# Kernel tuning notes

Measured on AMD Instinct MI355X. Metric: run time of the kernel, lower is better.

## Reference

```python
import jax, jax.numpy as jnp
import numpy as np

B, T, C, H = 2, 2048, 2048, 16
HD = C // H  # 128
WINDOW = 2048


def setup_inputs() -> dict:
    key = jax.random.key(0)
    k0, k1, k2 = jax.random.split(key, 3)
    s = 0.02  # GPT-2 style init scale
    return {
        "x": jax.random.normal(k0, (B, T, C), jnp.float32),
        "w_attn": jax.random.normal(k1, (3 * C, C), jnp.float32) * s,
        "b_attn": jnp.zeros((3 * C,), jnp.float32),
        "w_proj": jax.random.normal(k2, (C, C), jnp.float32) * s,
        "b_proj": jnp.zeros((C,), jnp.float32),
    }


def reference(x, w_attn, b_attn, w_proj, b_proj):
    Bb, Tt, Cc = x.shape
    # fused qkv projection (torch Linear: y = x @ W^T + b)
    qkv = x @ w_attn.T + b_attn                       # [B, T, 3C]
    q, k, v = jnp.split(qkv, 3, axis=2)

    def to_heads(t):
        return t.reshape(Bb, Tt, H, HD).transpose(0, 2, 1, 3)  # [B, H, T, HD]

    q, k, v = to_heads(q), to_heads(k), to_heads(v)
    K = k.shape[2]  # kv length (== T, no past_kv)

    attn = jnp.einsum('bhqd,bhkd->bhqk', q, k) / jnp.sqrt(jnp.float32(HD))
    # Faithful to source: mask[:, :, T-1:T, :K] — single tril row T-1 broadcast
    # over all query positions (for prefill K==T this row is all ones).
    mask_row = jnp.arange(K) <= (Tt - 1)              # [K] bool
    attn = jnp.where(mask_row[None, None, None, :], attn, -jnp.inf)
    weights = jax.nn.softmax(attn, axis=-1)            # [B, H, T, K]
    # dropout p=0.0 (eval): identity
    ctx = jnp.einsum('bhqk,bhkd->bhqd', weights, v)    # [B, H, T, HD]
    ctx = ctx.transpose(0, 2, 1, 3).reshape(Bb, Tt, Cc)
    out = ctx @ w_proj.T + b_proj                      # [B, T, C]
    return (out, k, v)  # (context, present_kv)
```

## Files before the change

kernel.cpp:

```cpp
#include <hip/hip_runtime.h>
#include <hip/hip_bf16.h>
#include <cstdint>
#include <cstddef>
#include <cmath>

typedef __attribute__((ext_vector_type(8))) short short8;
typedef __attribute__((ext_vector_type(4))) short bf16x4;
typedef __attribute__((ext_vector_type(4))) float f32x4;

static constexpr int BB = 2, T = 2048, C = 2048, H = 16, HD = 128;
static constexpr int M = BB * T;
static constexpr size_t BTC = (size_t)BB * T * C;

__device__ __forceinline__ short f2bf(float f) {
    union { float f; uint32_t u; } v; v.f = f;
    uint32_t u = v.u;
    uint32_t r = (u + 0x7fffu + ((u >> 16) & 1u)) >> 16;
    return (short)r;
}

__device__ __forceinline__ short f2bf_fast(float f) {
    __hip_bfloat16 h = __float2bfloat16(f);
    return *reinterpret_cast<short*>(&h);
}

__device__ __forceinline__ void gl_lds16(const void* g, void* l) {
    __builtin_amdgcn_global_load_lds(
        (const __attribute__((address_space(1))) unsigned int*)g,
        (__attribute__((address_space(3))) unsigned int*)l, 16, 0, 0);
}

__global__ void cvt_bf16(const float* __restrict__ in, short* __restrict__ out, int n) {
    int i = (blockIdx.x * 256 + threadIdx.x) * 8;
    if (i >= n) return;
    float4 a = *(const float4*)(in + i);
    float4 b = *(const float4*)(in + i + 4);
    short8 o;
    o[0] = f2bf(a.x); o[1] = f2bf(a.y); o[2] = f2bf(a.z); o[3] = f2bf(a.w);
    o[4] = f2bf(b.x); o[5] = f2bf(b.y); o[6] = f2bf(b.z); o[7] = f2bf(b.w);
    *(short8*)(out + i) = o;
}

__launch_bounds__(512, 2)
__global__ void gemm_qkv(const short* __restrict__ A, const short* __restrict__ Bw,
                         const float* __restrict__ bias, float* __restrict__ outF,
                         short* __restrict__ q_ws, short* __restrict__ k_ws) {
    extern __shared__ char lds[];
    constexpr int K = 2048, NKT = K / 64;
    constexpr int BUFSZ = 65536;

    int bid = blockIdx.x;
    int swz = (bid & 7) * 48 + (bid >> 3);
    int by = swz / 24, bx = swz % 24;
    int row0 = by * 256, col0 = bx * 256;

    int t = threadIdx.x, w = t >> 6, l = t & 63;
    int lr = l & 15, lg = l >> 4;
    int wr = w >> 2, wc = w & 3;

    const char* srcb[8];
    int dstoff[8];
#pragma unroll
    for (int c = 0; c < 8; c++) {
        bool isA = c < 4;
        int coff = (isA ? c : c - 4) * 8192 + t * 16;
        int row = coff >> 7;
        int colb = (coff & 127) ^ ((row & 7) << 4);
        srcb[c] = isA ? (const char*)A + (size_t)(row0 + row) * (K * 2) + colb
                      : (const char*)Bw + (size_t)(col0 + row) * (K * 2) + colb;
        dstoff[c] = (isA ? 0 : 32768) + coff;
    }

    f32x4 acc[8][4] = {};

#pragma unroll
    for (int c = 0; c < 8; c++) gl_lds16(srcb[c], lds + dstoff[c]);
#pragma unroll
    for (int c = 0; c < 8; c++) gl_lds16(srcb[c] + 128, lds + BUFSZ + dstoff[c]);
    asm volatile("s_waitcnt vmcnt(8)" ::: "memory");
    __builtin_amdgcn_s_barrier();

    for (int kt = 0; kt < NKT; kt++) {
        char* base = lds + (kt & 1) * BUFSZ;
        const char* Bbase = base + 32768;
        int koff = (kt + 2) * 128;
        bool pf = (kt + 2 < NKT);

        short8 bfr[4][2];
#pragma unroll
        for (int p = 0; p < 4; p++) {
            short8 af[2][2];
#pragma unroll
            for (int mi2 = 0; mi2 < 2; mi2++) {
                int row = wr * 128 + p * 32 + mi2 * 16 + lr;
#pragma unroll
                for (int ks = 0; ks < 2; ks++)
                    af[mi2][ks] = *(const short8*)(base + row * 128 +
                                  ((ks * 64 + lg * 16) ^ ((row & 7) << 4)));
            }
            if (p == 0) {
#pragma unroll
                for (int ni = 0; ni < 4; ni++) {
                    int row = wc * 64 + ni * 16 + lr;
#pragma unroll
                    for (int ks = 0; ks < 2; ks++)
                        bfr[ni][ks] = *(const short8*)(Bbase + row * 128 +
                                      ((ks * 64 + lg * 16) ^ ((row & 7) << 4)));
                }
            }
            __builtin_amdgcn_s_barrier();
            __builtin_amdgcn_s_setprio(1);
#pragma unroll
            for (int ks = 0; ks < 2; ks++)
#pragma unroll
                for (int mi2 = 0; mi2 < 2; mi2++)
#pragma unroll
                    for (int ni = 0; ni < 4; ni++)
                        acc[p * 2 + mi2][ni] = __builtin_amdgcn_mfma_f32_16x16x32_bf16(
                            af[mi2][ks], bfr[ni][ks], acc[p * 2 + mi2][ni], 0, 0, 0);
            __builtin_amdgcn_s_setprio(0);
            __builtin_amdgcn_s_barrier();

            if (pf) {
                if (p == 0) { gl_lds16(srcb[4] + koff, base + dstoff[4]);
                              gl_lds16(srcb[5] + koff, base + dstoff[5]); }
                if (p == 1) { gl_lds16(srcb[0] + koff, base + dstoff[0]);
                              gl_lds16(srcb[2] + koff, base + dstoff[2]); }
                if (p == 2) { gl_lds16(srcb[6] + koff, base + dstoff[6]);
                              gl_lds16(srcb[7] + koff, base + dstoff[7]); }
                if (p == 3) { gl_lds16(srcb[1] + koff, base + dstoff[1]);
                              gl_lds16(srcb[3] + koff, base + dstoff[3]); }
            }
            if (p == 3) {
                if (pf) asm volatile("s_waitcnt vmcnt(8)" ::: "memory");
                else    asm volatile("s_waitcnt vmcnt(0)" ::: "memory");
                __builtin_amdgcn_s_barrier();
            }
        }
    }

#pragma unroll
    for (int mi = 0; mi < 8; mi++) {
        int gr0 = row0 + wr * 128 + mi * 16 + lg * 4;
#pragma unroll
        for (int ni = 0; ni < 4; ni++) {
            int gc = col0 + wc * 64 + ni * 16 + lr;
            float bv = bias[gc];
            int sec = gc >> 11, cc = gc & 2047;
            int h = cc >> 7, d = cc & 127;
#pragma unroll
            for (int r = 0; r < 4; r++) {
                float val = acc[mi][ni][r] + bv;
                int gr = gr0 + r;
                int b = gr >> 11, tt = gr & 2047;
                size_t idx = ((size_t)(b * H + h) * T + tt) * HD + d;
                if (sec == 0) {
                    q_ws[idx] = f2bf(val);
                } else if (sec == 1) {
                    outF[BTC + idx] = val;
                    k_ws[idx] = f2bf(val);
                } else {
                    outF[2 * BTC + idx] = val;
                }
            }
        }
    }
}

template<int NI, int EPI, int NBX>
__launch_bounds__(512, 2)
__global__ void gemm8p(const short* __restrict__ A, const short* __restrict__ Bw,
                       const float* __restrict__ bias, float* __restrict__ outF,
                       short* __restrict__ q_ws, short* __restrict__ k_ws, int Ndim) {
    extern __shared__ char lds[];
    constexpr int K = 2048, NKT = K / 64;
    constexpr int NCH = 4 + NI;
    constexpr int BUFSZ = 32768 + NI * 8192;

    int bid = blockIdx.x;
    int nwg = gridDim.x;
    int swz = (bid & 7) * (nwg >> 3) + (bid >> 3);
    int by = swz / NBX, bx = swz % NBX;
    int row0 = by * 256, col0 = bx * (NI * 64);

    int t = threadIdx.x, w = t >> 6, l = t & 63;
    int lr = l & 15, lg = l >> 4;
    int wr = w >> 2, wc = w & 3;

    const char* srcb[NCH];
    int dstoff[NCH];
#pragma unroll
    for (int c = 0; c < NCH; c++) {
        bool isA = c < 4;
        int coff = (isA ? c : c - 4) * 8192 + t * 16;
        int row = coff >> 7;
        int colb = (coff & 127) ^ ((row & 7) << 4);
        srcb[c] = isA ? (const char*)A + (size_t)(row0 + row) * (K * 2) + colb
                      : (const char*)Bw + (size_t)(col0 + row) * (K * 2) + colb;
        dstoff[c] = (isA ? 0 : 32768) + coff;
    }

    f32x4 acc[8][NI] = {};

#pragma unroll
    for (int c = 0; c < NCH; c++) gl_lds16(srcb[c], lds + dstoff[c]);
#pragma unroll
    for (int c = 0; c < NCH; c++) gl_lds16(srcb[c] + 128, lds + BUFSZ + dstoff[c]);
    asm volatile("s_waitcnt vmcnt(%0)" :: "n"(NCH) : "memory");
    __builtin_amdgcn_s_barrier();

    for (int kt = 0; kt < NKT; kt++) {
        char* base = lds + (kt & 1) * BUFSZ;
        const char* Bbase = base + 32768;
        int koff = (kt + 2) * 128;
        bool pf = (kt + 2 < NKT);

        short8 bfr[NI][2];
#pragma unroll
        for (int p = 0; p < 4; p++) {
            short8 af[2][2];
#pragma unroll
            for (int mi2 = 0; mi2 < 2; mi2++) {
                int row = wr * 128 + p * 32 + mi2 * 16 + lr;
#pragma unroll
                for (int ks = 0; ks < 2; ks++)
                    af[mi2][ks] = *(const short8*)(base + row * 128 +
                                  ((ks * 64 + lg * 16) ^ ((row & 7) << 4)));
            }
            if (p == 0) {
#pragma unroll
                for (int ni = 0; ni < NI; ni++) {
                    int row = wc * (NI * 16) + ni * 16 + lr;
#pragma unroll
                    for (int ks = 0; ks < 2; ks++)
                        bfr[ni][ks] = *(const short8*)(Bbase + row * 128 +
                                      ((ks * 64 + lg * 16) ^ ((row & 7) << 4)));
                }
            }
            __builtin_amdgcn_s_barrier();
            __builtin_amdgcn_s_setprio(1);
#pragma unroll
            for (int ks = 0; ks < 2; ks++)
#pragma unroll
                for (int mi2 = 0; mi2 < 2; mi2++)
#pragma unroll
                    for (int ni = 0; ni < NI; ni++)
                        acc[p * 2 + mi2][ni] = __builtin_amdgcn_mfma_f32_16x16x32_bf16(
                            af[mi2][ks], bfr[ni][ks], acc[p * 2 + mi2][ni], 0, 0, 0);
            __builtin_amdgcn_s_setprio(0);
            __builtin_amdgcn_s_barrier();

            if (p == 0 && pf) {
#pragma unroll
                for (int c = 4; c < NCH; c++) gl_lds16(srcb[c] + koff, base + dstoff[c]);
            }
            if (p == 1 && pf) {
                gl_lds16(srcb[0] + koff, base + dstoff[0]);
                gl_lds16(srcb[2] + koff, base + dstoff[2]);
            }
            if (p == 3) {
                if (pf) {
                    gl_lds16(srcb[1] + koff, base + dstoff[1]);
                    gl_lds16(srcb[3] + koff, base + dstoff[3]);
                    asm volatile("s_waitcnt vmcnt(%0)" :: "n"(NCH) : "memory");
                } else {
                    asm volatile("s_waitcnt vmcnt(0)" ::: "memory");
                }
                __builtin_amdgcn_s_barrier();
            }
        }
    }

#pragma unroll
    for (int mi = 0; mi < 8; mi++) {
        int gr0 = row0 + wr * 128 + mi * 16 + lg * 4;
#pragma unroll
        for (int ni = 0; ni < NI; ni++) {
            int gc = col0 + wc * (NI * 16) + ni * 16 + lr;
            float bv = bias[gc];
#pragma unroll
            for (int r = 0; r < 4; r++)
                outF[(size_t)(gr0 + r) * Ndim + gc] = acc[mi][ni][r] + bv;
        }
    }
}

__global__ void vtrans(const float* __restrict__ vin, short* __restrict__ vT) {
    __shared__ float tile[64 * 65];
    int blk = blockIdx.x;
    int bh = blk >> 6, rem = blk & 63;
    int t0 = (rem >> 1) * 64, d0 = (rem & 1) * 64;
    const float* src = vin + (size_t)bh * T * HD;
    short* dst = vT + (size_t)bh * HD * T;
    int t = threadIdx.x;
#pragma unroll
    for (int i = 0; i < 16; i++) {
        int idx = i * 256 + t;
        int r = idx >> 6, c = idx & 63;
        tile[r * 65 + c] = src[(size_t)(t0 + r) * HD + d0 + c];
    }
    __syncthreads();
#pragma unroll
    for (int i = 0; i < 16; i++) {
        int idx = i * 256 + t;
        int rd = idx >> 6, cc = idx & 63;
        dst[(size_t)(d0 + rd) * T + t0 + cc] = f2bf(tile[cc * 65 + rd]);
    }
}

__launch_bounds__(256, 2)
__global__ void attn_fwd(const short* __restrict__ q_ws, const short* __restrict__ k_ws,
                         const short* __restrict__ vT_ws, short* __restrict__ ctx) {
    __shared__ __attribute__((aligned(16))) char K_lds[2][64 * 256];
    __shared__ __attribute__((aligned(16))) char VT_lds[2][128 * 128];
    __shared__ __attribute__((aligned(16))) char P_lds[4][16 * 128];

    int bid = blockIdx.x;
    int blk = (bid & 7) * 64 + (bid >> 3);
    int bh = blk >> 4;
    int q0 = (blk & 15) * 128;
    int b = bh >> 4, h = bh & 15;
    int t = threadIdx.x, w = t >> 6, l = t & 63;
    int lr = l & 15, lg = l >> 4;
    int sw = (lr & 7) << 4;

    short8 qf[2][4];
#pragma unroll
    for (int qt = 0; qt < 2; qt++) {
        const short* Qp = q_ws + ((size_t)bh * T + q0 + w * 32 + qt * 16 + lr) * HD;
#pragma unroll
        for (int c = 0; c < 4; c++) qf[qt][c] = *(const short8*)(Qp + c * 32 + lg * 8);
    }

    const char* Kp = (const char*)(k_ws + (size_t)bh * T * HD);
    const short* VTp = vT_ws + (size_t)bh * HD * T;
    char* Pc = P_lds[w];

    const float SC = 0.12753123813884803f;
    float m[2] = {-INFINITY, -INFINITY}, lsum[2] = {0.f, 0.f};
    f32x4 acc[2][8] = {};

    auto STAGE = [&](int kt, int bsel) {
#pragma unroll
        for (int i = 0; i < 4; i++) {
            int off = i * 4096 + t * 16;
            int swzK = off ^ (((off >> 8) & 7) << 4);
            gl_lds16(Kp + (size_t)kt * 16384 + swzK, K_lds[bsel] + off);
            int swzV = off ^ (((off >> 7) & 7) << 4);
            int row = swzV >> 7, cole = (swzV & 127) >> 1;
            gl_lds16(VTp + (size_t)row * T + kt * 64 + cole, VT_lds[bsel] + off);
        }
    };

    STAGE(0, 0);
    asm volatile("s_waitcnt vmcnt(0)" ::: "memory");
    __syncthreads();

    for (int kt = 0; kt < T / 64; kt++) {
        int cur = kt & 1;
        if (kt + 1 < T / 64) STAGE(kt + 1, cur ^ 1);
        const char* Kc = K_lds[cur];
        const char* Vc = VT_lds[cur];

        f32x4 sacc[2][4] = {};
#pragma unroll
        for (int kj = 0; kj < 4; kj++) {
            int rowb = (kj * 16 + lr) * 256;
#pragma unroll
            for (int c = 0; c < 4; c++) {
                short8 kf = *(const short8*)(Kc + ((rowb + c * 64 + lg * 16) ^ sw));
                sacc[0][kj] = __builtin_amdgcn_mfma_f32_16x16x32_bf16(kf, qf[0][c], sacc[0][kj], 0, 0, 0);
                sacc[1][kj] = __builtin_amdgcn_mfma_f32_16x16x32_bf16(kf, qf[1][c], sacc[1][kj], 0, 0, 0);
            }
        }

#pragma unroll
        for (int qt = 0; qt < 2; qt++) {
            float t0 = fmaxf(fmaxf(sacc[qt][0][0], sacc[qt][0][1]), fmaxf(sacc[qt][0][2], sacc[qt][0][3]));
            float t1 = fmaxf(fmaxf(sacc[qt][1][0], sacc[qt][1][1]), fmaxf(sacc[qt][1][2], sacc[qt][1][3]));
            float t2 = fmaxf(fmaxf(sacc[qt][2][0], sacc[qt][2][1]), fmaxf(sacc[qt][2][2], sacc[qt][2][3]));
            float t3 = fmaxf(fmaxf(sacc[qt][3][0], sacc[qt][3][1]), fmaxf(sacc[qt][3][2], sacc[qt][3][3]));
            float xm = fmaxf(fmaxf(t0, t1), fmaxf(t2, t3)) * SC;
            xm = fmaxf(xm, __shfl_xor(xm, 16));
            xm = fmaxf(xm, __shfl_xor(xm, 32));

            if (!__all(xm <= m[qt] + 8.0f)) {
                float mn = fmaxf(m[qt], xm);
                float al = __builtin_exp2f(m[qt] - mn);
                m[qt] = mn;
                lsum[qt] *= al;
                float ar[4];
#pragma unroll
                for (int r = 0; r < 4; r++) ar[r] = __shfl(al, lg * 4 + r);
#pragma unroll
                for (int nj = 0; nj < 8; nj++)
#pragma unroll
                    for (int r = 0; r < 4; r++) acc[qt][nj][r] *= ar[r];
            }

            float s0 = 0.f;
#pragma unroll
            for (int kj = 0; kj < 4; kj++) {
                bf16x4 pk;
#pragma unroll
                for (int r = 0; r < 4; r++) {
                    float pv = __builtin_exp2f(__builtin_fmaf(sacc[qt][kj][r], SC, -m[qt]));
                    s0 += pv;
                    pk[r] = f2bf_fast(pv);
                }
                *(bf16x4*)(Pc + ((lr * 128 + kj * 32 + lg * 8) ^ sw)) = pk;
            }
            s0 += __shfl_xor(s0, 16);
            s0 += __shfl_xor(s0, 32);
            lsum[qt] += s0;

            asm volatile("s_waitcnt lgkmcnt(0)" ::: "memory");

#pragma unroll
            for (int c2 = 0; c2 < 2; c2++) {
                short8 pf2 = *(const short8*)(Pc + ((lr * 128 + c2 * 64 + lg * 16) ^ sw));
#pragma unroll
                for (int nj = 0; nj < 8; nj++) {
                    short8 vf = *(const short8*)(Vc + (((nj * 16 + lr) * 128 + c2 * 64 + lg * 16) ^ sw));
                    acc[qt][nj] = __builtin_amdgcn_mfma_f32_16x16x32_bf16(pf2, vf, acc[qt][nj], 0, 0, 0);
                }
            }
        }

        asm volatile("s_waitcnt vmcnt(0)" ::: "memory");
        __syncthreads();
    }

#pragma unroll
    for (int qt = 0; qt < 2; qt++)
#pragma unroll
        for (int r = 0; r < 4; r++) {
            float rs = __shfl(lsum[qt], lg * 4 + r);
            float inv = 1.0f / rs;
            int tq = q0 + w * 32 + qt * 16 + lg * 4 + r;
            size_t base = ((size_t)b * T + tq) * C + h * HD;
#pragma unroll
            for (int nj = 0; nj < 8; nj++)
                ctx[base + nj * 16 + lr] = f2bf_fast(acc[qt][nj][r] * inv);
        }
}

extern "C" void kernel_launch(void* const* d_in, const int* in_sizes, int n_in,
                              void* d_out, int out_size, void* d_ws, size_t ws_size,
                              hipStream_t stream) {
    const float* x      = (const float*)d_in[0];
    const float* w_attn = (const float*)d_in[1];
    const float* b_attn = (const float*)d_in[2];
    const float* w_proj = (const float*)d_in[3];
    const float* b_proj = (const float*)d_in[4];
    float* out = (float*)d_out;

    char* ws = (char*)d_ws;
    short* x_bf  = (short*)ws;
    short* wp_bf = (short*)ws;
    short* wa_bf = (short*)(ws + 16777216);
    short* ctx   = (short*)(ws + 16777216);
    short* vT    = (short*)(ws + 41943040);

    short* q_ws = (short*)d_out;
    short* k_ws = (short*)d_out + BTC;

    hipFuncSetAttribute((const void*)gemm_qkv,
                        hipFuncAttributeMaxDynamicSharedMemorySize, 131072);
    hipFuncSetAttribute((const void*)gemm8p<2, 1, 16>,
                        hipFuncAttributeMaxDynamicSharedMemorySize, 98304);

    cvt_bf16<<<4096, 256, 0, stream>>>(x, x_bf, (int)BTC);
    cvt_bf16<<<6144, 256, 0, stream>>>(w_attn, wa_bf, 3 * C * C);

    gemm_qkv<<<384, 512, 131072, stream>>>(x_bf, wa_bf, b_attn, out, q_ws, k_ws);

    vtrans<<<2048, 256, 0, stream>>>(out + 2 * BTC, vT);
    cvt_bf16<<<2048, 256, 0, stream>>>(w_proj, wp_bf, C * C);

    attn_fwd<<<512, 256, 0, stream>>>(q_ws, k_ws, vT, ctx);

    gemm8p<2, 1, 16><<<256, 512, 98304, stream>>>(ctx, wp_bf, b_proj, out, nullptr, nullptr, 2048);
}
```

Baseline: 307.7 us.

## Retile QKV GEMM to 256x192 with 512 blocks and merge input conversions

Changes the QKV GEMM tile from 256x256 (384 blocks) to 256x192 (512 blocks), giving exactly two blocks per CU on 256 CUs instead of a partial wave. Block IDs are remapped so each group of eight shares rows and columns for L2 reuse. The per-phase barriers and staggered prefetches are replaced by a single prefetch and barrier pair per k-tile, which cuts synchronisation but may hurt overlap. The two fp32-to-bf16 conversion launches for x and w_attn are merged into one kernel to save a launch.

```diff
diff --git a/kernel.cpp b/kernel.cpp
--- a/kernel.cpp
+++ b/kernel.cpp
@@ -41,52 +41,68 @@
     *(short8*)(out + i) = o;
 }
 
+__global__ void cvt_qkv_in(const float* __restrict__ x, const float* __restrict__ wa,
+                           short* __restrict__ xb, short* __restrict__ wab) {
+    int i = (blockIdx.x * 256 + threadIdx.x) * 8;
+    const float* src;
+    short* dst;
+    if (i < (int)BTC) { src = x + i; dst = xb + i; }
+    else { src = wa + (i - (int)BTC); dst = wab + (i - (int)BTC); }
+    float4 a = *(const float4*)(src);
+    float4 b = *(const float4*)(src + 4);
+    short8 o;
+    o[0] = f2bf(a.x); o[1] = f2bf(a.y); o[2] = f2bf(a.z); o[3] = f2bf(a.w);
+    o[4] = f2bf(b.x); o[5] = f2bf(b.y); o[6] = f2bf(b.z); o[7] = f2bf(b.w);
+    *(short8*)(dst) = o;
+}
+
 __launch_bounds__(512, 2)
-__global__ void gemm_qkv(const short* __restrict__ A, const short* __restrict__ Bw,
-                         const float* __restrict__ bias, float* __restrict__ outF,
-                         short* __restrict__ q_ws, short* __restrict__ k_ws) {
+__global__ void gemm_qkv256(const short* __restrict__ A, const short* __restrict__ Bw,
+                            const float* __restrict__ bias, float* __restrict__ outF,
+                            short* __restrict__ q_ws, short* __restrict__ k_ws) {
     extern __shared__ char lds[];
     constexpr int K = 2048, NKT = K / 64;
-    constexpr int BUFSZ = 65536;
+    constexpr int BUFSZ = 57344;
 
     int bid = blockIdx.x;
-    int swz = (bid & 7) * 48 + (bid >> 3);
-    int by = swz / 24, bx = swz % 24;
-    int row0 = by * 256, col0 = bx * 256;
+    int g = bid & 7, j = bid >> 3;
+    int by = (g & 1) * 8 + (j >> 3);
+    int bx = (g >> 1) * 8 + (j & 7);
+    int row0 = by * 256, col0 = bx * 192;
 
     int t = threadIdx.x, w = t >> 6, l = t & 63;
     int lr = l & 15, lg = l >> 4;
     int wr = w >> 2, wc = w & 3;
 
-    const char* srcb[8];
-    int dstoff[8];
-#pragma unroll
-    for (int c = 0; c < 8; c++) {
+    const char* Ab = (const char*)A;
+    const char* Bb = (const char*)Bw;
+    const char* srcb[7];
+    int dstoff[7];
+#pragma unroll
+    for (int c = 0; c < 7; c++) {
         bool isA = c < 4;
         int coff = (isA ? c : c - 4) * 8192 + t * 16;
         int row = coff >> 7;
         int colb = (coff & 127) ^ ((row & 7) << 4);
-        srcb[c] = isA ? (const char*)A + (size_t)(row0 + row) * (K * 2) + colb
-                      : (const char*)Bw + (size_t)(col0 + row) * (K * 2) + colb;
+        srcb[c] = isA ? Ab + (size_t)(row0 + row) * (K * 2) + colb
+                      : Bb + (size_t)(col0 + row) * (K * 2) + colb;
         dstoff[c] = (isA ? 0 : 32768) + coff;
     }
 
-    f32x4 acc[8][4] = {};
-
-#pragma unroll
-    for (int c = 0; c < 8; c++) gl_lds16(srcb[c], lds + dstoff[c]);
-#pragma unroll
-    for (int c = 0; c < 8; c++) gl_lds16(srcb[c] + 128, lds + BUFSZ + dstoff[c]);
-    asm volatile("s_waitcnt vmcnt(8)" ::: "memory");
+    f32x4 acc[8][3] = {};
+
+#pragma unroll
+    for (int c = 0; c < 7; c++) gl_lds16(srcb[c], lds + dstoff[c]);
+#pragma unroll
+    for (int c = 0; c < 7; c++) gl_lds16(srcb[c] + 128, lds + BUFSZ + dstoff[c]);
+    asm volatile("s_waitcnt vmcnt(7)" ::: "memory");
     __builtin_amdgcn_s_barrier();
 
     for (int kt = 0; kt < NKT; kt++) {
-        char* base = lds + (kt & 1) * BUFSZ;
-        const char* Bbase = base + 32768;
-        int koff = (kt + 2) * 128;
-        bool pf = (kt + 2 < NKT);
-
-        short8 bfr[4][2];
+        const char* Abase = lds + (kt & 1) * BUFSZ;
+        const char* Bbase = Abase + 32768;
+
+        short8 bfr[3][2];
 #pragma unroll
         for (int p = 0; p < 4; p++) {
             short8 af[2][2];
@@ -95,56 +111,50 @@
                 int row = wr * 128 + p * 32 + mi2 * 16 + lr;
 #pragma unroll
                 for (int ks = 0; ks < 2; ks++)
-                    af[mi2][ks] = *(const short8*)(base + row * 128 +
+                    af[mi2][ks] = *(const short8*)(Abase + row * 128 +
                                   ((ks * 64 + lg * 16) ^ ((row & 7) << 4)));
             }
             if (p == 0) {
 #pragma unroll
-                for (int ni = 0; ni < 4; ni++) {
-                    int row = wc * 64 + ni * 16 + lr;
+                for (int ni = 0; ni < 3; ni++) {
+                    int row = wc * 48 + ni * 16 + lr;
 #pragma unroll
                     for (int ks = 0; ks < 2; ks++)
                         bfr[ni][ks] = *(const short8*)(Bbase + row * 128 +
                                       ((ks * 64 + lg * 16) ^ ((row & 7) << 4)));
                 }
             }
-            __builtin_amdgcn_s_barrier();
             __builtin_amdgcn_s_setprio(1);
 #pragma unroll
             for (int ks = 0; ks < 2; ks++)
 #pragma unroll
                 for (int mi2 = 0; mi2 < 2; mi2++)
 #pragma unroll
-                    for (int ni = 0; ni < 4; ni++)
+                    for (int ni = 0; ni < 3; ni++)
                         acc[p * 2 + mi2][ni] = __builtin_amdgcn_mfma_f32_16x16x32_bf16(
                             af[mi2][ks], bfr[ni][ks], acc[p * 2 + mi2][ni], 0, 0, 0);
             __builtin_amdgcn_s_setprio(0);
-            __builtin_amdgcn_s_barrier();
-
-            if (pf) {
-                if (p == 0) { gl_lds16(srcb[4] + koff, base + dstoff[4]);
-                              gl_lds16(srcb[5] + koff, base + dstoff[5]); }
-                if (p == 1) { gl_lds16(srcb[0] + koff, base + dstoff[0]);
-                              gl_lds16(srcb[2] + koff, base + dstoff[2]); }
-                if (p == 2) { gl_lds16(srcb[6] + koff, base + dstoff[6]);
-                              gl_lds16(srcb[7] + koff, base + dstoff[7]); }
-                if (p == 3) { gl_lds16(srcb[1] + koff, base + dstoff[1]);
-                              gl_lds16(srcb[3] + koff, base + dstoff[3]); }
-            }
-            if (p == 3) {
-                if (pf) asm volatile("s_waitcnt vmcnt(8)" ::: "memory");
-                else    asm volatile("s_waitcnt vmcnt(0)" ::: "memory");
-                __builtin_amdgcn_s_barrier();
-            }
-        }
+        }
+
+        __builtin_amdgcn_s_barrier();
+        if (kt + 2 < NKT) {
+            int koff = (kt + 2) * 128;
+            char* dbase = lds + (kt & 1) * BUFSZ;
+#pragma unroll
+            for (int c = 0; c < 7; c++) gl_lds16(srcb[c] + koff, dbase + dstoff[c]);
+            asm volatile("s_waitcnt vmcnt(7)" ::: "memory");
+        } else {
+            asm volatile("s_waitcnt vmcnt(0)" ::: "memory");
+        }
+        __builtin_amdgcn_s_barrier();
     }
 
 #pragma unroll
     for (int mi = 0; mi < 8; mi++) {
         int gr0 = row0 + wr * 128 + mi * 16 + lg * 4;
 #pragma unroll
-        for (int ni = 0; ni < 4; ni++) {
-            int gc = col0 + wc * 64 + ni * 16 + lr;
+        for (int ni = 0; ni < 3; ni++) {
+            int gc = col0 + wc * 48 + ni * 16 + lr;
             float bv = bias[gc];
             int sec = gc >> 11, cc = gc & 2047;
             int h = cc >> 7, d = cc & 127;
@@ -171,7 +181,7 @@
 __launch_bounds__(512, 2)
 __global__ void gemm8p(const short* __restrict__ A, const short* __restrict__ Bw,
                        const float* __restrict__ bias, float* __restrict__ outF,
-                       short* __restrict__ q_ws, short* __restrict__ k_ws, int Ndim) {
+                       int Ndim) {
     extern __shared__ char lds[];
     constexpr int K = 2048, NKT = K / 64;
     constexpr int NCH = 4 + NI;
@@ -465,20 +475,19 @@
     short* q_ws = (short*)d_out;
     short* k_ws = (short*)d_out + BTC;
 
-    hipFuncSetAttribute((const void*)gemm_qkv,
-                        hipFuncAttributeMaxDynamicSharedMemorySize, 131072);
+    hipFuncSetAttribute((const void*)gemm_qkv256,
+                        hipFuncAttributeMaxDynamicSharedMemorySize, 114688);
     hipFuncSetAttribute((const void*)gemm8p<2, 1, 16>,
                         hipFuncAttributeMaxDynamicSharedMemorySize, 98304);
 
-    cvt_bf16<<<4096, 256, 0, stream>>>(x, x_bf, (int)BTC);
-    cvt_bf16<<<6144, 256, 0, stream>>>(w_attn, wa_bf, 3 * C * C);
-
-    gemm_qkv<<<384, 512, 131072, stream>>>(x_bf, wa_bf, b_attn, out, q_ws, k_ws);
+    cvt_qkv_in<<<10240, 256, 0, stream>>>(x, w_attn, x_bf, wa_bf);
+
+    gemm_qkv256<<<512, 512, 114688, stream>>>(x_bf, wa_bf, b_attn, out, q_ws, k_ws);
 
     vtrans<<<2048, 256, 0, stream>>>(out + 2 * BTC, vT);
     cvt_bf16<<<2048, 256, 0, stream>>>(w_proj, wp_bf, C * C);
 
     attn_fwd<<<512, 256, 0, stream>>>(q_ws, k_ws, vT, ctx);
 
-    gemm8p<2, 1, 16><<<256, 512, 98304, stream>>>(ctx, wp_bf, b_proj, out, nullptr, nullptr, 2048);
-}
+    gemm8p<2, 1, 16><<<256, 512, 98304, stream>>>(ctx, wp_bf, b_proj, out, 2048);
+}
```

Result: faster. 289.5 us (-5.9%).
